# Optimization experiments

Measured on AMD Instinct MI355X. Metric: run time of the kernel, lower is better.

## Reference

```python
import jax, jax.numpy as jnp
import numpy as np
import math

B, S, D, H = 8, 1024, 1024, 16
HD = D // H  # head_dim = 64

def setup_inputs() -> dict:
    key = jax.random.key(0)
    ks = jax.random.split(key, 5)
    x = jax.random.normal(ks[0], (B, S, D), dtype=jnp.float32)
    mask = jnp.zeros((S, S), dtype=jnp.float32)
    # torch Linear: weight shape (out, in), y = x @ W.T + b
    Wqkv = jax.random.normal(ks[1], (3 * D, D), dtype=jnp.float32) * (1.0 / math.sqrt(D))
    bqkv = jax.random.normal(ks[2], (3 * D,), dtype=jnp.float32) * 0.01
    Wo = jax.random.normal(ks[3], (D, D), dtype=jnp.float32) * (1.0 / math.sqrt(D))
    bo = jax.random.normal(ks[4], (D,), dtype=jnp.float32) * 0.01
    return {"x": x, "mask": mask, "Wqkv": Wqkv, "bqkv": bqkv, "Wo": Wo, "bo": bo}

def reference(x, mask, Wqkv, bqkv, Wo, bo):
    b, s, d = x.shape
    qkv = x @ Wqkv.T + bqkv                       # (B,S,3D)
    qkv = qkv.reshape(b, s, H, 3 * HD).transpose(0, 2, 1, 3)  # (B,H,S,3hd)
    q, k, v = jnp.split(qkv, 3, axis=-1)          # each (B,H,S,hd)
    scaled = jnp.einsum('bhqd,bhkd->bhqk', q, k) / math.sqrt(HD)
    # original permutes to (H,B,S,S), adds mask, permutes back
    scaled = (scaled.transpose(1, 0, 2, 3) + mask).transpose(1, 0, 2, 3)
    attention = jax.nn.softmax(scaled, axis=-1)   # (B,H,S,S)
    values = jnp.einsum('bhqk,bhkd->bhqd', attention, v)  # (B,H,S,hd)
    # FAITHFUL to original bug: reshape (B,H,S,hd) -> (B,S,D) without head transpose
    values = values.reshape(b, s, d)
    out = values @ Wo.T + bo
    return out
```

## Files before the change

### kernel.cpp

```cpp
#include <hip/hip_runtime.h>
#include <math.h>


typedef __attribute__((ext_vector_type(8))) short short8v;
typedef __attribute__((ext_vector_type(4))) float floatx4;

__device__ inline unsigned short f2bf(float f) {
    return __builtin_bit_cast(unsigned short, (__bf16)f);
}
__device__ inline float bf2f(unsigned short u) {
    return (float)__builtin_bit_cast(__bf16, u);
}

__device__ inline void gload_lds16(const void* g, void* l) {
    __builtin_amdgcn_global_load_lds((const __attribute__((address_space(1))) void*)g,
                                     (__attribute__((address_space(3))) void*)l,
                                     16, 0, 0);
}

__global__ __launch_bounds__(256) void conv_split(
    const float* __restrict__ W, unsigned short* __restrict__ Wp)
{
    int i = (blockIdx.x * 256 + threadIdx.x) * 4;
    int row = i >> 10, c = i & 1023;
    float4 v = *(const float4*)&W[i];
    float f[4] = {v.x, v.y, v.z, v.w};
    unsigned short hs[4], ls[4];
#pragma unroll
    for (int j = 0; j < 4; ++j) {
        hs[j] = f2bf(f[j]);
        ls[j] = f2bf(f[j] - bf2f(hs[j]));
    }
    ushort4 h4 = {hs[0], hs[1], hs[2], hs[3]};
    ushort4 l4 = {ls[0], ls[1], ls[2], ls[3]};
    size_t base = (size_t)row * 2048;
    *(ushort4*)&Wp[base + c] = h4;
    *(ushort4*)&Wp[base + 1024 + c] = l4;
}

__global__ __launch_bounds__(256) void gemm1_qkv(
    const unsigned short* __restrict__ Xp,
    const unsigned short* __restrict__ Wp,
    const float* __restrict__ bias,
    unsigned short* __restrict__ qkv_hi,
    unsigned short* __restrict__ qk_lo)
{
    __shared__ unsigned short As[128 * 32];
    __shared__ unsigned short Bs[128 * 32];

    const int tid = threadIdx.x;
    const int lane = tid & 63, wave = tid >> 6;
    const int wr = wave >> 1, wc = wave & 1;
    const int wg = blockIdx.y * 24 + blockIdx.x;
    const int swz = (wg & 7) * 192 + (wg >> 3);
    const int bm = (swz / 24) * 128, bn = (swz % 24) * 128;

    floatx4 acc[4][4] = {};

    for (int k0 = 0; k0 < 3072; k0 += 32) {
        const int region = k0 >> 10;
        const int acol = ((region == 2) ? 1024 : 0) + (k0 & 1023);
        const int bcol = ((region == 1) ? 1024 : 0) + (k0 & 1023);

        __syncthreads();

#pragma unroll
        for (int c = 0; c < 2; ++c) {
            int o = wave * 2048 + c * 1024 + lane * 16;
            int row = o >> 6, ce = (o & 63) >> 1;
            gload_lds16(Xp + (size_t)(bm + row) * 2048 + acol + ce, (char*)As + o);
            gload_lds16(Wp + (size_t)(bn + row) * 2048 + bcol + ce, (char*)Bs + o);
        }

        __syncthreads();

        short8v af[4], bf[4];
#pragma unroll
        for (int m = 0; m < 4; ++m)
            af[m] = *(short8v*)((char*)As + (wr * 64 + m * 16 + (lane & 15)) * 64 + (lane >> 4) * 16);
#pragma unroll
        for (int n = 0; n < 4; ++n)
            bf[n] = *(short8v*)((char*)Bs + (wc * 64 + n * 16 + (lane & 15)) * 64 + (lane >> 4) * 16);
#pragma unroll
        for (int m = 0; m < 4; ++m)
#pragma unroll
            for (int n = 0; n < 4; ++n)
                acc[m][n] = __builtin_amdgcn_mfma_f32_16x16x32_bf16(af[m], bf[n], acc[m][n], 0, 0, 0);
    }

#pragma unroll
    for (int n = 0; n < 4; ++n) {
        int col = bn + wc * 64 + n * 16 + (lane & 15);
        float bb = bias[col];
        int hh = col / 192, within = col % 192;
#pragma unroll
        for (int m = 0; m < 4; ++m)
#pragma unroll
            for (int j = 0; j < 4; ++j) {
                int row = bm + wr * 64 + m * 16 + (lane >> 4) * 4 + j;
                float val = acc[m][n][j] + bb;
                if (within < 64) {
                    float vs = val * 0.125f;
                    unsigned short h = f2bf(vs);
                    qkv_hi[(size_t)row * 3072 + col] = h;
                    qk_lo[(size_t)row * 2048 + hh * 128 + within] = f2bf(vs - bf2f(h));
                } else if (within < 128) {
                    unsigned short h = f2bf(val);
                    qkv_hi[(size_t)row * 3072 + col] = h;
                    qk_lo[(size_t)row * 2048 + hh * 128 + within] = f2bf(val - bf2f(h));
                } else {
                    qkv_hi[(size_t)row * 3072 + col] = f2bf(val);
                }
            }
    }
}

#define QP 200
#define VP 72
#define MP 65

__global__ __launch_bounds__(256) void attn_mfma2(
    const unsigned short* __restrict__ qkv_hi,
    const unsigned short* __restrict__ qk_lo,
    const float* __restrict__ mask,
    unsigned short* __restrict__ V2p)
{
    __shared__ unsigned short Ks[64 * QP];
    __shared__ unsigned short VT[64 * VP];
    __shared__ unsigned short Ps[64 * VP];
    __shared__ float msT[64 * MP];

    const int tid = threadIdx.x, lane = tid & 63, w = tid >> 6;
    const int i = lane & 15, lg = lane >> 4;
    const int qb = blockIdx.x, h = blockIdx.y, b = blockIdx.z;
    const size_t hi_base = (size_t)b * 1024 * 3072;
    const size_t lo_base = (size_t)b * 1024 * 2048;
    const int hq = h * 192, hk = h * 192 + 64, hv = h * 192 + 128;
    const int lq = h * 128, lk = h * 128 + 64;

    short8v qf[6];
    {
        const int qrow = qb * 64 + w * 16 + i;
#pragma unroll
        for (int ks = 0; ks < 6; ++ks) {
            int c = ks * 32 + lg * 8;
            const unsigned short* src = (c < 128)
                ? qkv_hi + hi_base + (size_t)qrow * 3072 + hq + (c & 63)
                : qk_lo + lo_base + (size_t)qrow * 2048 + lq + (c - 128);
            qf[ks] = *(const short8v*)src;
        }
    }

    short8v kreg[6], vreg[2];
    float4 mreg[4];
    const int kr = tid >> 2, d0 = (tid & 3) * 16;

    auto load_ch = [&](int ch) {
#pragma unroll
        for (int p = 0; p < 6; ++p) {
            int c = p * 256 + tid;
            int r = c / 24, k8 = (c % 24) * 8;
            const unsigned short* s;
            if (k8 < 64)       s = qkv_hi + hi_base + (size_t)(ch * 64 + r) * 3072 + hk + k8;
            else if (k8 < 128) s = qk_lo + lo_base + (size_t)(ch * 64 + r) * 2048 + lk + (k8 - 64);
            else               s = qkv_hi + hi_base + (size_t)(ch * 64 + r) * 3072 + hk + (k8 - 128);
            kreg[p] = *(const short8v*)s;
        }
        const unsigned short* vsrc = qkv_hi + hi_base + (size_t)(ch * 64 + kr) * 3072 + hv + d0;
        vreg[0] = *(const short8v*)vsrc;
        vreg[1] = *(const short8v*)(vsrc + 8);
#pragma unroll
        for (int p = 0; p < 4; ++p) {
            int idx = p * 256 + tid;
            mreg[p] = *(const float4*)&mask[(size_t)(qb * 64 + (idx >> 4)) * 1024 + ch * 64 + (idx & 15) * 4];
        }
    };

    auto write_ch = [&]() {
#pragma unroll
        for (int p = 0; p < 6; ++p) {
            int c = p * 256 + tid;
            int r = c / 24, k8 = (c % 24) * 8;
            *(short8v*)&Ks[r * QP + k8] = kreg[p];
        }
        {
            unsigned kh = kr >> 3, klo = kr & 7;
#pragma unroll
            for (int j = 0; j < 16; ++j) {
                unsigned short vv = (j < 8) ? (unsigned short)vreg[0][j] : (unsigned short)vreg[1][j - 8];
                int d = d0 + j;
                VT[d * VP + ((kh ^ ((d >> 3) & 7)) * 8 + klo)] = vv;
            }
        }
#pragma unroll
        for (int p = 0; p < 4; ++p) {
            int idx = p * 256 + tid;
            int q = idx >> 4, k4 = (idx & 15) * 4;
            msT[(k4 + 0) * MP + q] = mreg[p].x;
            msT[(k4 + 1) * MP + q] = mreg[p].y;
            msT[(k4 + 2) * MP + q] = mreg[p].z;
            msT[(k4 + 3) * MP + q] = mreg[p].w;
        }
    };

    load_ch(0);
    float m_run = -3e30f, l_run = 0.f;
    floatx4 accv[4] = {};
    const unsigned qsw = ((w * 16 + i) >> 2) & 7;

    for (int ch = 0; ch < 16; ++ch) {
        __syncthreads();
        write_ch();
        __syncthreads();
        if (ch < 15) load_ch(ch + 1);

        floatx4 sc[4] = {};
#pragma unroll
        for (int ks = 0; ks < 6; ++ks) {
#pragma unroll
            for (int n = 0; n < 4; ++n) {
                short8v kf = *(const short8v*)&Ks[(n * 16 + i) * QP + ks * 32 + lg * 8];
                sc[n] = __builtin_amdgcn_mfma_f32_16x16x32_bf16(kf, qf[ks], sc[n], 0, 0, 0);
            }
        }

        float sv[4][4];
        float cmax = -3e30f;
#pragma unroll
        for (int n = 0; n < 4; ++n)
#pragma unroll
            for (int r = 0; r < 4; ++r) {
                float val = sc[n][r] + msT[(n * 16 + lg * 4 + r) * MP + w * 16 + i];
                sv[n][r] = val;
                cmax = fmaxf(cmax, val);
            }
        cmax = fmaxf(cmax, __shfl_xor(cmax, 16));
        cmax = fmaxf(cmax, __shfl_xor(cmax, 32));

        float mnew = fmaxf(m_run, cmax);
        float fct = __expf(m_run - mnew);
        m_run = mnew;
        float rsum = 0.f;
        float pv[4][4];
#pragma unroll
        for (int n = 0; n < 4; ++n)
#pragma unroll
            for (int r = 0; r < 4; ++r) {
                float pp = __expf(sv[n][r] - mnew);
                pv[n][r] = pp;
                rsum += pp;
            }
        rsum += __shfl_xor(rsum, 16);
        rsum += __shfl_xor(rsum, 32);
        l_run = l_run * fct + rsum;

        float fr[4];
#pragma unroll
        for (int r = 0; r < 4; ++r) fr[r] = __shfl(fct, lg * 4 + r);
#pragma unroll
        for (int n = 0; n < 4; ++n)
#pragma unroll
            for (int r = 0; r < 4; ++r) accv[n][r] *= fr[r];

#pragma unroll
        for (int n = 0; n < 4; ++n)
#pragma unroll
            for (int u = 0; u < 2; ++u) {
                unsigned kh = 2 * n + (lg >> 1);
                unsigned klo = 4 * (lg & 1) + 2 * u;
                unsigned col = (kh ^ qsw) * 8 + klo;
                unsigned pk = (unsigned)f2bf(pv[n][2 * u]) | ((unsigned)f2bf(pv[n][2 * u + 1]) << 16);
                *(unsigned*)&Ps[(w * 16 + i) * VP + col] = pk;
            }

#pragma unroll
        for (int ks = 0; ks < 2; ++ks) {
            short8v pf = *(const short8v*)&Ps[(w * 16 + i) * VP + ((ks * 4 + lg) ^ qsw) * 8];
#pragma unroll
            for (int n = 0; n < 4; ++n) {
                int d = n * 16 + i;
                short8v vf = *(const short8v*)&VT[d * VP + (((ks * 4 + lg) ^ ((d >> 3) & 7)) * 8)];
                accv[n] = __builtin_amdgcn_mfma_f32_16x16x32_bf16(pf, vf, accv[n], 0, 0, 0);
            }
        }
    }

    float linv = 1.f / l_run;
    float lr[4];
#pragma unroll
    for (int r = 0; r < 4; ++r) lr[r] = __shfl(linv, lg * 4 + r);
#pragma unroll
    for (int r = 0; r < 4; ++r) {
        int s_ = qb * 64 + w * 16 + lg * 4 + r;
        size_t row2 = (size_t)(b * 1024 + h * 64 + (s_ >> 4)) * 2048;
        int colh = (s_ & 15) * 64;
#pragma unroll
        for (int n = 0; n < 4; ++n) {
            int d = n * 16 + i;
            float val = accv[n][r] * lr[r];
            unsigned short hh2 = f2bf(val);
            V2p[row2 + colh + d] = hh2;
            V2p[row2 + 1024 + colh + d] = f2bf(val - bf2f(hh2));
        }
    }
}

__global__ __launch_bounds__(256) void gemm2_out(
    const unsigned short* __restrict__ V2,
    const unsigned short* __restrict__ Wop,
    const float* __restrict__ bias,
    float* __restrict__ Out)
{
    __shared__ unsigned short As[128 * 32];
    __shared__ unsigned short Bs[128 * 32];

    const int tid = threadIdx.x;
    const int lane = tid & 63, wave = tid >> 6;
    const int wr = wave >> 1, wc = wave & 1;
    const int wg = blockIdx.y * 8 + blockIdx.x;
    const int swz = (wg & 7) * 64 + (wg >> 3);
    const int bm = (swz / 8) * 128, bn = (swz % 8) * 128;

    floatx4 acc[4][4] = {};

    for (int k0 = 0; k0 < 3072; k0 += 32) {
        const int region = k0 >> 10;
        const int acol = ((region == 2) ? 1024 : 0) + (k0 & 1023);
        const int bcol = ((region == 1) ? 1024 : 0) + (k0 & 1023);

        __syncthreads();

#pragma unroll
        for (int c = 0; c < 2; ++c) {
            int o = wave * 2048 + c * 1024 + lane * 16;
            int row = o >> 6, ce = (o & 63) >> 1;
            gload_lds16(V2 + (size_t)(bm + row) * 2048 + acol + ce, (char*)As + o);
            gload_lds16(Wop + (size_t)(bn + row) * 2048 + bcol + ce, (char*)Bs + o);
        }

        __syncthreads();

        short8v af[4], bf[4];
#pragma unroll
        for (int m = 0; m < 4; ++m)
            af[m] = *(short8v*)((char*)As + (wr * 64 + m * 16 + (lane & 15)) * 64 + (lane >> 4) * 16);
#pragma unroll
        for (int n = 0; n < 4; ++n)
            bf[n] = *(short8v*)((char*)Bs + (wc * 64 + n * 16 + (lane & 15)) * 64 + (lane >> 4) * 16);
#pragma unroll
        for (int m = 0; m < 4; ++m)
#pragma unroll
            for (int n = 0; n < 4; ++n)
                acc[m][n] = __builtin_amdgcn_mfma_f32_16x16x32_bf16(af[m], bf[n], acc[m][n], 0, 0, 0);
    }

#pragma unroll
    for (int n = 0; n < 4; ++n) {
        int col = bn + wc * 64 + n * 16 + (lane & 15);
        float bb = bias[col];
#pragma unroll
        for (int m = 0; m < 4; ++m)
#pragma unroll
            for (int j = 0; j < 4; ++j) {
                int row = bm + wr * 64 + m * 16 + (lane >> 4) * 4 + j;
                Out[(size_t)row * 1024 + col] = acc[m][n][j] + bb;
            }
    }
}

extern "C" void kernel_launch(void* const* d_in, const int* in_sizes, int n_in,
                              void* d_out, int out_size, void* d_ws, size_t ws_size,
                              hipStream_t stream)
{
    const float* x    = (const float*)d_in[0];
    const float* mask = (const float*)d_in[1];
    const float* Wqkv = (const float*)d_in[2];
    const float* bqkv = (const float*)d_in[3];
    const float* Wo   = (const float*)d_in[4];
    const float* bo   = (const float*)d_in[5];
    float* out = (float*)d_out;

    char* w = (char*)d_ws;
    unsigned short* Xp     = (unsigned short*)w;
    unsigned short* V2p    = (unsigned short*)w;
    unsigned short* qkv_hi = (unsigned short*)(w + 33554432);
    unsigned short* qk_lo  = (unsigned short*)(w + 83886080);
    unsigned short* Wp     = (unsigned short*)(w + 117440512);
    unsigned short* Wop    = (unsigned short*)(w + 117440512);

    conv_split<<<8192, 256, 0, stream>>>(x, Xp);
    conv_split<<<3072, 256, 0, stream>>>(Wqkv, Wp);

    gemm1_qkv<<<dim3(24, 64), 256, 0, stream>>>(Xp, Wp, bqkv, qkv_hi, qk_lo);

    conv_split<<<1024, 256, 0, stream>>>(Wo, Wop);

    attn_mfma2<<<dim3(16, 16, 8), 256, 0, stream>>>(qkv_hi, qk_lo, mask, V2p);

    gemm2_out<<<dim3(8, 64), 256, 0, stream>>>(V2p, Wop, bo, out);
}
```

Measured before the change: 530.5 us.

## Pre-transpose mask, load it to registers, lazily rescale softmax, set MFMA priority

New measurement: 523.2 us. About the same (-1.4%).

```diff
diff --git a/kernel.cpp b/kernel.cpp
--- a/kernel.cpp
+++ b/kernel.cpp
@@ -36,6 +36,21 @@
     size_t base = (size_t)row * 2048;
     *(ushort4*)&Wp[base + c] = h4;
     *(ushort4*)&Wp[base + 1024 + c] = l4;
+}
+
+__global__ __launch_bounds__(256) void transpose_mask(
+    const float* __restrict__ m, float* __restrict__ mt)
+{
+    __shared__ float t[64][65];
+    const int bx = blockIdx.x * 64, by = blockIdx.y * 64;
+    const int tx = threadIdx.x & 63, r0 = (threadIdx.x >> 6) * 16;
+#pragma unroll
+    for (int r = 0; r < 16; ++r)
+        t[r0 + r][tx] = m[(size_t)(by + r0 + r) * 1024 + bx + tx];
+    __syncthreads();
+#pragma unroll
+    for (int r = 0; r < 16; ++r)
+        mt[(size_t)(bx + r0 + r) * 1024 + by + tx] = t[tx][r0 + r];
 }
 
 __global__ __launch_bounds__(256) void gemm1_qkv(
@@ -117,26 +132,25 @@
 
 #define QP 200
 #define VP 72
-#define MP 65
-
-__global__ __launch_bounds__(256) void attn_mfma2(
+
+__global__ __launch_bounds__(256) void attn_mfma3(
     const unsigned short* __restrict__ qkv_hi,
     const unsigned short* __restrict__ qk_lo,
-    const float* __restrict__ mask,
+    const float* __restrict__ maskT,
     unsigned short* __restrict__ V2p)
 {
     __shared__ unsigned short Ks[64 * QP];
     __shared__ unsigned short VT[64 * VP];
     __shared__ unsigned short Ps[64 * VP];
-    __shared__ float msT[64 * MP];
 
     const int tid = threadIdx.x, lane = tid & 63, w = tid >> 6;
     const int i = lane & 15, lg = lane >> 4;
     const int qb = blockIdx.x, h = blockIdx.y, b = blockIdx.z;
     const size_t hi_base = (size_t)b * 1024 * 3072;
     const size_t lo_base = (size_t)b * 1024 * 2048;
-    const int hq = h * 192, hk = h * 192 + 64, hv = h * 192 + 128;
+    const int hk = h * 192 + 64, hv = h * 192 + 128;
     const int lq = h * 128, lk = h * 128 + 64;
+    const int hq = h * 192;
 
     short8v qf[6];
     {
@@ -152,10 +166,10 @@
     }
 
     short8v kreg[6], vreg[2];
-    float4 mreg[4];
+    float mreg[16];
     const int kr = tid >> 2, d0 = (tid & 3) * 16;
 
-    auto load_ch = [&](int ch) {
+    auto load_kv = [&](int ch) {
 #pragma unroll
         for (int p = 0; p < 6; ++p) {
             int c = p * 256 + tid;
@@ -169,11 +183,15 @@
         const unsigned short* vsrc = qkv_hi + hi_base + (size_t)(ch * 64 + kr) * 3072 + hv + d0;
         vreg[0] = *(const short8v*)vsrc;
         vreg[1] = *(const short8v*)(vsrc + 8);
-#pragma unroll
-        for (int p = 0; p < 4; ++p) {
-            int idx = p * 256 + tid;
-            mreg[p] = *(const float4*)&mask[(size_t)(qb * 64 + (idx >> 4)) * 1024 + ch * 64 + (idx & 15) * 4];
-        }
+    };
+
+    auto load_mask = [&](int ch) {
+#pragma unroll
+        for (int n = 0; n < 4; ++n)
+#pragma unroll
+            for (int r = 0; r < 4; ++r)
+                mreg[n * 4 + r] = maskT[(size_t)(ch * 64 + n * 16 + lg * 4 + r) * 1024
+                                        + qb * 64 + w * 16 + i];
     };
 
     auto write_ch = [&]() {
@@ -192,18 +210,10 @@
                 VT[d * VP + ((kh ^ ((d >> 3) & 7)) * 8 + klo)] = vv;
             }
         }
-#pragma unroll
-        for (int p = 0; p < 4; ++p) {
-            int idx = p * 256 + tid;
-            int q = idx >> 4, k4 = (idx & 15) * 4;
-            msT[(k4 + 0) * MP + q] = mreg[p].x;
-            msT[(k4 + 1) * MP + q] = mreg[p].y;
-            msT[(k4 + 2) * MP + q] = mreg[p].z;
-            msT[(k4 + 3) * MP + q] = mreg[p].w;
-        }
     };
 
-    load_ch(0);
+    load_kv(0);
+    load_mask(0);
     float m_run = -3e30f, l_run = 0.f;
     floatx4 accv[4] = {};
     const unsigned qsw = ((w * 16 + i) >> 2) & 7;
@@ -212,9 +222,10 @@
         __syncthreads();
         write_ch();
         __syncthreads();
-        if (ch < 15) load_ch(ch + 1);
+        if (ch < 15) load_kv(ch + 1);
 
         floatx4 sc[4] = {};
+        __builtin_amdgcn_s_setprio(1);
 #pragma unroll
         for (int ks = 0; ks < 6; ++ks) {
 #pragma unroll
@@ -223,6 +234,7 @@
                 sc[n] = __builtin_amdgcn_mfma_f32_16x16x32_bf16(kf, qf[ks], sc[n], 0, 0, 0);
             }
         }
+        __builtin_amdgcn_s_setprio(0);
 
         float sv[4][4];
         float cmax = -3e30f;
@@ -230,37 +242,42 @@
         for (int n = 0; n < 4; ++n)
 #pragma unroll
             for (int r = 0; r < 4; ++r) {
-                float val = sc[n][r] + msT[(n * 16 + lg * 4 + r) * MP + w * 16 + i];
+                float val = sc[n][r] + mreg[n * 4 + r];
                 sv[n][r] = val;
                 cmax = fmaxf(cmax, val);
             }
         cmax = fmaxf(cmax, __shfl_xor(cmax, 16));
         cmax = fmaxf(cmax, __shfl_xor(cmax, 32));
 
-        float mnew = fmaxf(m_run, cmax);
-        float fct = __expf(m_run - mnew);
-        m_run = mnew;
+        if (!__all(cmax - m_run <= 8.f)) {
+            float mnew = fmaxf(m_run, cmax);
+            float fct = __expf(m_run - mnew);
+            m_run = mnew;
+            l_run *= fct;
+            float fr[4];
+#pragma unroll
+            for (int r = 0; r < 4; ++r) fr[r] = __shfl(fct, lg * 4 + r);
+#pragma unroll
+            for (int n = 0; n < 4; ++n)
+#pragma unroll
+                for (int r = 0; r < 4; ++r) accv[n][r] *= fr[r];
+        }
+
         float rsum = 0.f;
         float pv[4][4];
 #pragma unroll
         for (int n = 0; n < 4; ++n)
 #pragma unroll
             for (int r = 0; r < 4; ++r) {
-                float pp = __expf(sv[n][r] - mnew);
+                float pp = __expf(sv[n][r] - m_run);
                 pv[n][r] = pp;
                 rsum += pp;
             }
         rsum += __shfl_xor(rsum, 16);
         rsum += __shfl_xor(rsum, 32);
-        l_run = l_run * fct + rsum;
-
-        float fr[4];
-#pragma unroll
-        for (int r = 0; r < 4; ++r) fr[r] = __shfl(fct, lg * 4 + r);
-#pragma unroll
-        for (int n = 0; n < 4; ++n)
-#pragma unroll
-            for (int r = 0; r < 4; ++r) accv[n][r] *= fr[r];
+        l_run += rsum;
+
+        if (ch < 15) load_mask(ch + 1);
 
 #pragma unroll
         for (int n = 0; n < 4; ++n)
@@ -273,6 +290,7 @@
                 *(unsigned*)&Ps[(w * 16 + i) * VP + col] = pk;
             }
 
+        __builtin_amdgcn_s_setprio(1);
 #pragma unroll
         for (int ks = 0; ks < 2; ++ks) {
             short8v pf = *(const short8v*)&Ps[(w * 16 + i) * VP + ((ks * 4 + lg) ^ qsw) * 8];
@@ -283,6 +301,7 @@
                 accv[n] = __builtin_amdgcn_mfma_f32_16x16x32_bf16(pf, vf, accv[n], 0, 0, 0);
             }
         }
+        __builtin_amdgcn_s_setprio(0);
     }
 
     float linv = 1.f / l_run;
@@ -387,6 +406,7 @@
     unsigned short* qk_lo  = (unsigned short*)(w + 83886080);
     unsigned short* Wp     = (unsigned short*)(w + 117440512);
     unsigned short* Wop    = (unsigned short*)(w + 117440512);
+    float*          maskT  = (float*)(w + 117440512 + 4194304);
 
     conv_split<<<8192, 256, 0, stream>>>(x, Xp);
     conv_split<<<3072, 256, 0, stream>>>(Wqkv, Wp);
@@ -394,8 +414,9 @@
     gemm1_qkv<<<dim3(24, 64), 256, 0, stream>>>(Xp, Wp, bqkv, qkv_hi, qk_lo);
 
     conv_split<<<1024, 256, 0, stream>>>(Wo, Wop);
-
-    attn_mfma2<<<dim3(16, 16, 8), 256, 0, stream>>>(qkv_hi, qk_lo, mask, V2p);
+    transpose_mask<<<dim3(16, 16), 256, 0, stream>>>(mask, maskT);
+
+    attn_mfma3<<<dim3(16, 16, 8), 256, 0, stream>>>(qkv_hi, qk_lo, maskT, V2p);
 
     gemm2_out<<<dim3(8, 64), 256, 0, stream>>>(V2p, Wop, bo, out);
 }
```
